# Kernel tuning notes

Hardware: AMD Instinct MI355X
Metric: run time of the kernel (lower is better)

Reference implementation:

```python
import jax, jax.numpy as jnp
import numpy as np

B, D, K = 16384, 32, 128  # batch, cluster_dim, num_clusters


def setup_inputs() -> dict:
    key = jax.random.key(0)
    x = jax.random.normal(key, (B, D, K), dtype=jnp.float32)
    mu_0 = jnp.zeros((D, K), dtype=jnp.float32)                      # running mean buffer
    L_0 = jnp.broadcast_to(jnp.eye(D, dtype=jnp.float32), (K, D, D)) # running Cholesky buffer
    n_0 = jnp.ones((1,), dtype=jnp.float32)                          # running count
    return {"x": x, "mu_0": mu_0, "L_0": L_0, "n_0": n_0}


def reference(x, mu_0, L_0, n_0):
    # Training-mode forward of ClusterNorm1dv2.
    Bn = x.shape[0]
    eps_eye = jnp.eye(x.shape[1], dtype=x.dtype)
    n0 = n_0[0]
    x_mu = jnp.mean(x, axis=0)                         # [D, K]
    x_cnt = jnp.transpose(x - x_mu[None], (2, 1, 0))   # [K, D, B]
    C = jnp.einsum('kdb,keb->kde', x_cnt, x_cnt)       # [K, D, D] per-cluster scatter
    denom = n0 + Bn
    new_mu = (n0 * mu_0 + Bn * x_mu) / denom           # [D, K]
    x_d = jnp.transpose((x_mu - mu_0)[None], (2, 1, 0))  # [K, D, 1]
    new_cov = (jnp.einsum('kde,kfe->kdf', L_0, L_0) * (n0 / denom)
               + C / denom
               + jnp.einsum('kdo,keo->kde', x_d, x_d) * (n0 * Bn / denom ** 2))
    L = jnp.linalg.cholesky(new_cov + eps_eye)         # [K, D, D]
    xc = jnp.transpose(x - new_mu[None], (2, 1, 0))    # [K, D, B]
    Z = jax.scipy.linalg.solve_triangular(L, xc, lower=True)  # whitening solve
    return jnp.transpose(Z, (2, 1, 0))                 # [B, D, K]
```

## Files before the change

kernel.cpp:

```cpp
#include <hip/hip_runtime.h>

typedef __attribute__((ext_vector_type(4))) float f32x4;

#define NB 16384
#define ND 32
#define NK 128

template<int SP>
__device__ __forceinline__ void k1_body(const float* __restrict__ x,
                                        float* __restrict__ part,
                                        float* __restrict__ vs,
                                        int k0, int b0, int t) {
  constexpr int CL = 4*(SP+1);
  constexpr int CH = 4*(8-SP);
  const int sd = t >> 3, sj = t & 7;
  const int kl = t & 63;

  float aL[4][CL];
  float aH[4][CH];
  float ssum[8];
  #pragma unroll
  for (int r=0;r<4;r++){
    #pragma unroll
    for (int c=0;c<CL;c++) aL[r][c]=0.f;
    #pragma unroll
    for (int c=0;c<CH;c++) aH[r][c]=0.f;
  }
  #pragma unroll
  for (int i=0;i<8;i++) ssum[i]=0.f;

  for (int g=0; g<32; ++g) {
    #pragma unroll
    for (int s=0;s<2;s++){
      const int b = b0 + g*2 + s;
      const float* src = x + (b*ND + sd)*NK + k0 + 4*sj;
      const f32x4 A0 = *(const f32x4*)src;
      const f32x4 A1 = *(const f32x4*)(src+32);
      float* dst = vs + s*2304;
      #pragma unroll
      for (int i=0;i<4;i++){
        dst[(4*sj+i)*36 + sd]    = A0[i];
        dst[(4*sj+32+i)*36 + sd] = A1[i];
        ssum[i]   += A0[i];
        ssum[4+i] += A1[i];
      }
    }
    __syncthreads();
    #pragma unroll
    for (int s=0;s<2;s++){
      const float* row = vs + s*2304 + kl*36;
      f32x4 bv[8-SP];
      #pragma unroll
      for (int q=0;q<8-SP;q++) bv[q] = *(const f32x4*)(row + 4*q);
      #pragma unroll
      for (int r=0;r<4;r++){
        const float al = bv[SP][r];
        const float ah = bv[7-SP][r];
        #pragma unroll
        for (int q=0;q<=SP;q++){
          #pragma unroll
          for (int i=0;i<4;i++) aL[r][4*q+i] += al*bv[q][i];
        }
        #pragma unroll
        for (int q=0;q<8-SP;q++){
          #pragma unroll
          for (int i=0;i<4;i++) aH[r][4*q+i] += ah*bv[q][i];
        }
      }
    }
    __syncthreads();
  }

  float* pb = part + blockIdx.x*38912;
  #pragma unroll
  for (int r=0;r<4;r++){
    #pragma unroll
    for (int c=0;c<CL;c++)
      pb[(8*SP*(SP+1) + r*CL + c)*64 + kl] = aL[r][c];
    #pragma unroll
    for (int c=0;c<CH;c++)
      pb[(8*(7-SP)*(8-SP) + r*CH + c)*64 + kl] = aH[r][c];
  }
  #pragma unroll
  for (int i=0;i<4;i++){
    pb[(576+sd)*64 + 4*sj + i]      = ssum[i];
    pb[(576+sd)*64 + 32 + 4*sj + i] = ssum[4+i];
  }
}

__global__ __launch_bounds__(256, 2) void k1_scatter(const float* __restrict__ x,
                                                     float* __restrict__ part) {
  __shared__ float vs[2*2304];
  const int t = threadIdx.x;
  const int ktile = blockIdx.x & 1;
  const int chunk = blockIdx.x >> 1;
  const int k0 = ktile*64, b0 = chunk*64;
  switch (t>>6) {
    case 0:  k1_body<0>(x, part, vs, k0, b0, t); break;
    case 1:  k1_body<1>(x, part, vs, k0, b0, t); break;
    case 2:  k1_body<2>(x, part, vs, k0, b0, t); break;
    default: k1_body<3>(x, part, vs, k0, b0, t); break;
  }
}

__global__ void k2a_reduce(const float* __restrict__ part, float* __restrict__ sfin) {
  const int t = threadIdx.x;
  const int bx = blockIdx.x;
  const int h = bx & 1, ktile = (bx>>1)&1, vg = bx>>2;
  const int vidx = vg*4 + (t>>6);
  const int kl = t & 63;
  const float* p = part + ((size_t)(h*128)*2 + ktile)*38912 + vidx*64 + kl;
  float a0=0.f,a1=0.f,a2=0.f,a3=0.f;
  for (int c=0;c<128;c+=4){
    a0 += p[(size_t)(c+0)*77824];
    a1 += p[(size_t)(c+1)*77824];
    a2 += p[(size_t)(c+2)*77824];
    a3 += p[(size_t)(c+3)*77824];
  }
  sfin[h*77824 + vidx*128 + ktile*64 + kl] = (a0+a1)+(a2+a3);
}

__global__ void k2b_chol(const float* __restrict__ sfin,
                         const float* __restrict__ mu0,
                         const float* __restrict__ L0,
                         const float* __restrict__ n0p,
                         float* __restrict__ lpad,
                         float* __restrict__ nmu) {
  const int k = blockIdx.x;
  const int t = threadIdx.x;
  __shared__ float L0s[32*33];
  __shared__ float Am[32*33];
  __shared__ float xdl[32];
  __shared__ float dinv[32];
  const float n0 = n0p[0];
  const float denom = n0 + (float)NB;

  for (int idx = t; idx < 1024; idx += 256)
    L0s[(idx>>5)*33 + (idx&31)] = L0[k*1024 + idx];
  if (t < 32) {
    const float S  = sfin[(576+t)*128 + k] + sfin[77824 + (576+t)*128 + k];
    const float m0 = mu0[t*128 + k];
    nmu[t*128 + k] = (n0*m0 + S) / denom;
    xdl[t] = S*(1.0f/NB) - m0;
  }
  __syncthreads();

  const float c1 = n0/denom, c2 = 1.0f/denom;
  const float c3 = n0*(float)NB/(denom*denom);
  for (int idx = t; idx < 1024; idx += 256) {
    const int d = idx>>5, e = idx&31;
    const int dd = d>=e?d:e, ee = d>=e?e:d;
    const int R = dd>>2;
    const int vi = 8*R*(R+1) + (dd&3)*4*(R+1) + ee;
    const float M  = sfin[vi*128 + k]      + sfin[77824 + vi*128 + k];
    const float Sd = sfin[(576+d)*128 + k] + sfin[77824 + (576+d)*128 + k];
    const float Se = sfin[(576+e)*128 + k] + sfin[77824 + (576+e)*128 + k];
    const float C = M - Sd*Se*(1.0f/NB);
    float g = 0.f;
    #pragma unroll 8
    for (int f=0; f<32; f++) g += L0s[d*33+f]*L0s[e*33+f];
    float a = g*c1 + C*c2 + xdl[d]*xdl[e]*c3;
    if (d==e) a += 1.0f;
    Am[d*33+e] = a;
  }
  __syncthreads();

  for (int j=0;j<32;j++){
    float acc = 0.f;
    if (t < 32 && t >= j) {
      acc = Am[t*33+j];
      for (int e=0;e<j;e++) acc -= Am[t*33+e]*Am[j*33+e];
    }
    __syncthreads();
    if (t == j) {
      const float dj = sqrtf(acc);
      Am[j*33+j] = dj;
      dinv[j] = 1.0f/dj;
    }
    __syncthreads();
    if (t < 32 && t > j) Am[t*33+j] = acc*dinv[j];
    __syncthreads();
  }

  if (t < 32) {
    const int d = t;
    int rs = 0;
    for (int e=0;e<d;e++) rs += (e+3)>>2;
    rs *= 4;
    const int rl = ((d+3)>>2)*4;
    float* lp = lpad + k*576;
    for (int e=0;e<rl;e++) lp[rs+e] = (e<d) ? Am[d*33+e] : 0.f;
    lp[544+d] = dinv[d];
  }
}

__global__ __launch_bounds__(256, 2) void k3_whiten(const float* __restrict__ x,
                                                    const float* __restrict__ lpad,
                                                    const float* __restrict__ nmu,
                                                    float* __restrict__ out) {
  __shared__ float Lw[32*580];
  __shared__ float muL[32*32];
  const int t = threadIdx.x;
  const int bx = blockIdx.x;
  const int ktile = bx & 3;
  const int chunk = bx >> 2;
  const int k0 = ktile*32;

  {
    const f32x4* src = (const f32x4*)(lpad + (size_t)k0*576);
    #pragma unroll
    for (int q=0;q<18;q++){
      const int idx = t + q*256;
      const int row = idx/144, col = idx - row*144;
      *(f32x4*)(&Lw[row*580 + col*4]) = src[idx];
    }
    #pragma unroll
    for (int idx=t; idx<1024; idx+=256)
      muL[idx] = nmu[(idx>>5)*128 + k0 + (idx&31)];
  }
  __syncthreads();

  const int kl = t & 31;
  const int so = t >> 5;
  const float* Lrow = &Lw[kl*580];
  const int b0 = chunk*128;

  for (int it=0; it<4; ++it) {
    const int base = b0 + it*32 + so;
    const float* xa = x + (size_t)(base     )*4096 + k0 + kl;
    const float* xb = x + (size_t)(base +  8)*4096 + k0 + kl;
    const float* xc = x + (size_t)(base + 16)*4096 + k0 + kl;
    const float* xd = x + (size_t)(base + 24)*4096 + k0 + kl;
    float vA[32], vB[32], vC[32], vD[32];
    #pragma unroll
    for (int d=0; d<32; ++d) vA[d] = xa[d*128];
    #pragma unroll
    for (int d=0; d<32; ++d) vB[d] = xb[d*128];
    #pragma unroll
    for (int d=0; d<32; ++d) vC[d] = xc[d*128];
    #pragma unroll
    for (int d=0; d<32; ++d) vD[d] = xd[d*128];
    #pragma unroll
    for (int d=0; d<32; ++d) {
      const float m = muL[d*32 + kl];
      vA[d] -= m; vB[d] -= m; vC[d] -= m; vD[d] -= m;
    }
    int rs = 0;
    #pragma unroll
    for (int d=0; d<32; ++d) {
      float sA = vA[d], sB = vB[d], sC = vC[d], sD = vD[d];
      const int nq = (d+3)>>2;
      #pragma unroll
      for (int q=0; q<nq; ++q) {
        const f32x4 Lq = *(const f32x4*)(Lrow + rs + 4*q);
        sA -= Lq[0]*vA[4*q+0] + Lq[1]*vA[4*q+1] + Lq[2]*vA[4*q+2] + Lq[3]*vA[4*q+3];
        sB -= Lq[0]*vB[4*q+0] + Lq[1]*vB[4*q+1] + Lq[2]*vB[4*q+2] + Lq[3]*vB[4*q+3];
        sC -= Lq[0]*vC[4*q+0] + Lq[1]*vC[4*q+1] + Lq[2]*vC[4*q+2] + Lq[3]*vC[4*q+3];
        sD -= Lq[0]*vD[4*q+0] + Lq[1]*vD[4*q+1] + Lq[2]*vD[4*q+2] + Lq[3]*vD[4*q+3];
      }
      const float di = Lrow[544+d];
      vA[d] = sA*di; vB[d] = sB*di; vC[d] = sC*di; vD[d] = sD*di;
      rs += 4*nq;
    }
    float* oa = out + (size_t)(base     )*4096 + k0 + kl;
    float* ob = out + (size_t)(base +  8)*4096 + k0 + kl;
    float* oc = out + (size_t)(base + 16)*4096 + k0 + kl;
    float* od = out + (size_t)(base + 24)*4096 + k0 + kl;
    #pragma unroll
    for (int d=0; d<32; ++d) oa[d*128] = vA[d];
    #pragma unroll
    for (int d=0; d<32; ++d) ob[d*128] = vB[d];
    #pragma unroll
    for (int d=0; d<32; ++d) oc[d*128] = vC[d];
    #pragma unroll
    for (int d=0; d<32; ++d) od[d*128] = vD[d];
  }
}

extern "C" void kernel_launch(void* const* d_in, const int* in_sizes, int n_in,
                              void* d_out, int out_size, void* d_ws, size_t ws_size,
                              hipStream_t stream) {
  const float* x   = (const float*)d_in[0];
  const float* mu0 = (const float*)d_in[1];
  const float* L0  = (const float*)d_in[2];
  const float* n0  = (const float*)d_in[3];
  float* out  = (float*)d_out;
  float* part = out;
  float* sfin = out + 20971520;
  float* lpad = (float*)d_ws;
  float* nmu  = lpad + 128*576;

  k1_scatter<<<512, 256, 0, stream>>>(x, part);
  k2a_reduce<<<608, 256, 0, stream>>>(part, sfin);
  k2b_chol  <<<128, 256, 0, stream>>>(sfin, mu0, L0, n0, lpad, nmu);
  k3_whiten <<<512, 256, 0, stream>>>(x, lpad, nmu, out);
}
```

Baseline: 235.1 us.

## Prefetch scatter tiles with double-buffered LDS, halve k1 grid, remap whiten blocks

The scatter kernel now loads the next pair of batch rows into registers while the current pair is being accumulated. It double-buffers the shared tile so one barrier per iteration can be dropped, and it processes 128 batch rows per block with half as many blocks, which shrinks the partial-sum reduction. The whiten kernel remaps block indices so blocks running together touch different k-tiles, and it writes output with nontemporal stores. Risks are fewer blocks in flight for k1, higher register use from the prefetch buffers, and twice the LDS per block.

```diff
diff --git a/kernel.cpp b/kernel.cpp
--- a/kernel.cpp
+++ b/kernel.cpp
@@ -29,26 +29,41 @@
   #pragma unroll
   for (int i=0;i<8;i++) ssum[i]=0.f;
 
-  for (int g=0; g<32; ++g) {
+  const float* src0 = x + ((size_t)b0*ND + sd)*NK + k0 + 4*sj;
+
+  f32x4 rc[2][2], rn[2][2];
+  #pragma unroll
+  for (int s=0;s<2;s++){
+    const float* src = src0 + (size_t)s*4096;
+    rc[s][0] = *(const f32x4*)src;
+    rc[s][1] = *(const f32x4*)(src+32);
+  }
+
+  for (int g=0; g<64; ++g) {
+    if (g < 63) {
+      #pragma unroll
+      for (int s=0;s<2;s++){
+        const float* src = src0 + (size_t)(2*(g+1)+s)*4096;
+        rn[s][0] = *(const f32x4*)src;
+        rn[s][1] = *(const f32x4*)(src+32);
+      }
+    }
+    float* dstbuf = vs + (g&1)*4608;
     #pragma unroll
     for (int s=0;s<2;s++){
-      const int b = b0 + g*2 + s;
-      const float* src = x + (b*ND + sd)*NK + k0 + 4*sj;
-      const f32x4 A0 = *(const f32x4*)src;
-      const f32x4 A1 = *(const f32x4*)(src+32);
-      float* dst = vs + s*2304;
+      float* dst = dstbuf + s*2304;
       #pragma unroll
       for (int i=0;i<4;i++){
-        dst[(4*sj+i)*36 + sd]    = A0[i];
-        dst[(4*sj+32+i)*36 + sd] = A1[i];
-        ssum[i]   += A0[i];
-        ssum[4+i] += A1[i];
+        dst[(4*sj+i)*36 + sd]    = rc[s][0][i];
+        dst[(4*sj+32+i)*36 + sd] = rc[s][1][i];
+        ssum[i]   += rc[s][0][i];
+        ssum[4+i] += rc[s][1][i];
       }
     }
     __syncthreads();
     #pragma unroll
     for (int s=0;s<2;s++){
-      const float* row = vs + s*2304 + kl*36;
+      const float* row = dstbuf + s*2304 + kl*36;
       f32x4 bv[8-SP];
       #pragma unroll
       for (int q=0;q<8-SP;q++) bv[q] = *(const f32x4*)(row + 4*q);
@@ -68,10 +83,11 @@
         }
       }
     }
-    __syncthreads();
-  }
-
-  float* pb = part + blockIdx.x*38912;
+    #pragma unroll
+    for (int s=0;s<2;s++){ rc[s][0]=rn[s][0]; rc[s][1]=rn[s][1]; }
+  }
+
+  float* pb = part + (size_t)blockIdx.x*38912;
   #pragma unroll
   for (int r=0;r<4;r++){
     #pragma unroll
@@ -90,11 +106,11 @@
 
 __global__ __launch_bounds__(256, 2) void k1_scatter(const float* __restrict__ x,
                                                      float* __restrict__ part) {
-  __shared__ float vs[2*2304];
+  __shared__ float vs[2*4608];
   const int t = threadIdx.x;
   const int ktile = blockIdx.x & 1;
   const int chunk = blockIdx.x >> 1;
-  const int k0 = ktile*64, b0 = chunk*64;
+  const int k0 = ktile*64, b0 = chunk*128;
   switch (t>>6) {
     case 0:  k1_body<0>(x, part, vs, k0, b0, t); break;
     case 1:  k1_body<1>(x, part, vs, k0, b0, t); break;
@@ -109,9 +125,9 @@
   const int h = bx & 1, ktile = (bx>>1)&1, vg = bx>>2;
   const int vidx = vg*4 + (t>>6);
   const int kl = t & 63;
-  const float* p = part + ((size_t)(h*128)*2 + ktile)*38912 + vidx*64 + kl;
+  const float* p = part + ((size_t)(h*64)*2 + ktile)*38912 + vidx*64 + kl;
   float a0=0.f,a1=0.f,a2=0.f,a3=0.f;
-  for (int c=0;c<128;c+=4){
+  for (int c=0;c<64;c+=4){
     a0 += p[(size_t)(c+0)*77824];
     a1 += p[(size_t)(c+1)*77824];
     a2 += p[(size_t)(c+2)*77824];
@@ -202,8 +218,10 @@
   __shared__ float muL[32*32];
   const int t = threadIdx.x;
   const int bx = blockIdx.x;
-  const int ktile = bx & 3;
-  const int chunk = bx >> 2;
+  const int m = (bx >> 3) & 1;
+  const int u = ((bx >> 4) << 3) | (bx & 7);
+  const int ktile = ((u & 1) << 1) | m;
+  const int chunk = u >> 1;
   const int k0 = ktile*32;
 
   {
@@ -242,8 +260,8 @@
     for (int d=0; d<32; ++d) vD[d] = xd[d*128];
     #pragma unroll
     for (int d=0; d<32; ++d) {
-      const float m = muL[d*32 + kl];
-      vA[d] -= m; vB[d] -= m; vC[d] -= m; vD[d] -= m;
+      const float m2 = muL[d*32 + kl];
+      vA[d] -= m2; vB[d] -= m2; vC[d] -= m2; vD[d] -= m2;
     }
     int rs = 0;
     #pragma unroll
@@ -267,13 +285,13 @@
     float* oc = out + (size_t)(base + 16)*4096 + k0 + kl;
     float* od = out + (size_t)(base + 24)*4096 + k0 + kl;
     #pragma unroll
-    for (int d=0; d<32; ++d) oa[d*128] = vA[d];
-    #pragma unroll
-    for (int d=0; d<32; ++d) ob[d*128] = vB[d];
-    #pragma unroll
-    for (int d=0; d<32; ++d) oc[d*128] = vC[d];
-    #pragma unroll
-    for (int d=0; d<32; ++d) od[d*128] = vD[d];
+    for (int d=0; d<32; ++d) __builtin_nontemporal_store(vA[d], oa + d*128);
+    #pragma unroll
+    for (int d=0; d<32; ++d) __builtin_nontemporal_store(vB[d], ob + d*128);
+    #pragma unroll
+    for (int d=0; d<32; ++d) __builtin_nontemporal_store(vC[d], oc + d*128);
+    #pragma unroll
+    for (int d=0; d<32; ++d) __builtin_nontemporal_store(vD[d], od + d*128);
   }
 }
 
@@ -290,7 +308,7 @@
   float* lpad = (float*)d_ws;
   float* nmu  = lpad + 128*576;
 
-  k1_scatter<<<512, 256, 0, stream>>>(x, part);
+  k1_scatter<<<256, 256, 0, stream>>>(x, part);
   k2a_reduce<<<608, 256, 0, stream>>>(part, sfin);
   k2b_chol  <<<128, 256, 0, stream>>>(sfin, mu0, L0, n0, lpad, nmu);
   k3_whiten <<<512, 256, 0, stream>>>(x, lpad, nmu, out);
```

Result: slower. 259.6 us (+10.4%).
